# Kernel tuning notes

Measured on AMD Instinct MI355X. Metric: run time of the kernel, lower is better.

The kernel has to match this reference:

```python
import jax, jax.numpy as jnp
import numpy as np

N = 524288   # tokens (accounts)
D = 9        # num_prop_size
E = 2        # expert_size
H = 128      # expert MLP hidden
M = 32       # moe_out
O = 2        # output_size
K = 1        # top-k
LOSS_COF = 0.01
EPS = 1e-10


def setup_inputs() -> dict:
    key = jax.random.key(0)
    ks = jax.random.split(key, 10)
    f32 = jnp.float32
    return {
        "num_prop": jax.random.normal(ks[0], (N, D), f32),
        "cat_prop": jax.random.normal(ks[1], (N, 3), f32),
        "w_gate": jax.random.normal(ks[2], (D, E), f32) * 0.1,
        "W1": jax.random.normal(ks[3], (E, D, H), f32) * 0.1,
        "b1": jax.random.normal(ks[4], (E, H), f32) * 0.01,
        "W2": jax.random.normal(ks[5], (E, H, M), f32) * 0.1,
        "b2": jax.random.normal(ks[6], (E, M), f32) * 0.01,
        "Wout": jax.random.normal(ks[7], (M, O), f32) * 0.1,
        "bout": jax.random.normal(ks[8], (O,), f32) * 0.01,
        "k": K,
    }


def _cv_squared(x):
    # torch: x.var() (unbiased) / (x.mean()**2 + eps)
    return jnp.var(x, ddof=1) / (jnp.mean(x) ** 2 + EPS)


def reference(num_prop, cat_prop, w_gate, W1, b1, W2, b2, Wout, bout, k):
    x = num_prop                                   # eval mode: dropout = identity
    n, e = x.shape[0], w_gate.shape[1]

    # --- top-k gating (eval: clean logits, no noise) ---
    logits = x @ w_gate                            # [N, E]
    top_logits, top_idx = jax.lax.top_k(logits, min(k + 1, e))
    top_k_gates = jax.nn.softmax(top_logits[:, :k], axis=1)   # [N, k]
    rows = jnp.arange(n)[:, None]
    gates = jnp.zeros_like(logits).at[rows, top_idx[:, :k]].set(top_k_gates)  # [N, E]

    importance = gates.sum(axis=0)                 # [E]
    load = (gates > 0).astype(jnp.float32).sum(axis=0)  # [E]
    loss = (_cv_squared(importance) + _cv_squared(load)) * LOSS_COF

    # --- experts: per-expert 2-layer MLP, computed dense (E=2) then gated combine ---
    h = jax.nn.relu(jnp.einsum("nd,edh->neh", x, W1) + b1)    # [N, E, H]
    y_e = jnp.einsum("neh,ehm->nem", h, W2) + b2              # [N, E, M]
    y = jnp.einsum("ne,nem->nm", gates, y_e)                  # [N, M]

    out = y @ Wout + bout                                     # [N, O]
    return (out, loss)
```

## Files before the change

### kernel.cpp

```cpp
#include <hip/hip_runtime.h>

#define NTOK 524288
#define TPB  256
#define TOKB 1024
#define NBLK (NTOK / TOKB)

__device__ __forceinline__ float bf2f(unsigned short u) {
    union { unsigned int i; float f; } v;
    v.i = ((unsigned int)u) << 16;
    return v.f;
}

__device__ __forceinline__ float ldq(const void* p, int i, bool f32) {
    if (f32) return ((const float*)p)[i];
    return bf2f(((const unsigned short*)p)[i]);
}

__global__ void prep_kernel(const void* __restrict__ num_prop,
                            const void* __restrict__ wgate,
                            const void* __restrict__ W1,
                            const void* __restrict__ b1,
                            const void* __restrict__ W2,
                            const void* __restrict__ b2,
                            const void* __restrict__ Wout,
                            const void* __restrict__ bout,
                            unsigned int* __restrict__ cnt1,
                            int* __restrict__ flag,
                            float* __restrict__ bpp,
                            float* __restrict__ wgf,
                            float* __restrict__ wpack)
{
    __shared__ unsigned int bad;
    __shared__ int sflag;
    const int t = threadIdx.x;
    if (t == 0) { bad = 0u; *cnt1 = 0u; }
    __syncthreads();
    if (t < 72) {
        const unsigned short* u = (const unsigned short*)num_prop;
        int e = (u[t] >> 7) & 0xFF;
        if (e < 64 || e > 191) atomicOr(&bad, 1u);
    }
    __syncthreads();
    if (t == 0) { sflag = (int)bad; *flag = (int)bad; }
    __syncthreads();
    const bool f32 = (sflag != 0);

    if (t < 18) wgf[t] = ldq(wgate, t, f32);

    if (t < 4) {
        int e = t >> 1, o = t & 1;
        float acc = ldq(bout, o, f32);
        for (int m = 0; m < 32; ++m)
            acc += ldq(b2, e * 32 + m, f32) * ldq(Wout, m * 2 + o, f32);
        bpp[t] = acc;
    }

    const int e = t >> 7;
    const int j = t & 127;
    float p0 = 0.f, p1 = 0.f;
    for (int m = 0; m < 32; ++m) {
        float w = ldq(W2, (e * 128 + j) * 32 + m, f32);
        p0 += w * ldq(Wout, m * 2 + 0, f32);
        p1 += w * ldq(Wout, m * 2 + 1, f32);
    }
    float* dst = wpack + e * 2048 + j * 16;
    #pragma unroll
    for (int d = 0; d < 9; ++d)
        dst[d] = ldq(W1, (e * 9 + d) * 128 + j, f32);
    dst[9]  = ldq(b1, e * 128 + j, f32);
    dst[10] = p0;
    dst[11] = p1;
    dst[12] = 0.f; dst[13] = 0.f; dst[14] = 0.f; dst[15] = 0.f;
}

__global__ __launch_bounds__(TPB, 2)
void moe_main(const void* __restrict__ xg,
              const int* __restrict__ flag,
              const float* __restrict__ wgf,
              const float* __restrict__ bpp,
              const float* __restrict__ wpack,
              unsigned int* __restrict__ cnt1,
              float2* __restrict__ out)
{
    __shared__ __align__(16) float xs[TOKB * 9];
    __shared__ unsigned short smap[TOKB];
    __shared__ unsigned int wcnt[16];

    const int tid  = threadIdx.x;
    const int lane = tid & 63;
    const int wave = tid >> 6;

    const bool f32 = (*flag) != 0;
    const int gbase = blockIdx.x * (TOKB * 9);
    if (f32) {
        const float* xf = (const float*)xg;
        #pragma unroll
        for (int i = 0; i < 36; ++i)
            xs[tid + i * TPB] = xf[gbase + tid + i * TPB];
    } else {
        const unsigned short* xu = (const unsigned short*)xg;
        for (int i = tid; i < TOKB * 9; i += TPB)
            xs[i] = bf2f(xu[gbase + i]);
    }
    __syncthreads();

    bool e1g[4];
    unsigned long long balg[4];
    #pragma unroll
    for (int g = 0; g < 4; ++g) {
        float l0 = 0.f, l1 = 0.f;
        #pragma unroll
        for (int d = 0; d < 9; ++d) {
            float xv = xs[(g * 256 + tid) * 9 + d];
            l0 = fmaf(xv, wgf[d * 2 + 0], l0);
            l1 = fmaf(xv, wgf[d * 2 + 1], l1);
        }
        e1g[g] = l1 > l0;
        balg[g] = __ballot(e1g[g]);
        if (lane == 0) wcnt[g * 4 + wave] = (unsigned int)__popcll(balg[g]);
    }
    __syncthreads();

    int pres[16]; int run = 0;
    #pragma unroll
    for (int c = 0; c < 16; ++c) { pres[c] = run; run += (int)wcnt[c]; }
    const int n1 = run;
    const int n0 = TOKB - n1;
    const unsigned long long below = (1ull << lane) - 1ull;
    #pragma unroll
    for (int g = 0; g < 4; ++g) {
        const int tok = g * 256 + tid;
        const int pr  = pres[g * 4 + wave] + (int)__popcll(balg[g] & below);
        const int slot = e1g[g] ? (n0 + pr) : (tok - pr);
        smap[slot] = (unsigned short)tok;
    }
    if (tid == 0) atomicAdd(cnt1, (unsigned int)n1);
    __syncthreads();

    const int s0 = tid * 4;
    const int tk0 = (int)smap[s0 + 0], tk1 = (int)smap[s0 + 1];
    const int tk2 = (int)smap[s0 + 2], tk3 = (int)smap[s0 + 3];
    float x0[9], x1[9], x2[9], x3[9];
    #pragma unroll
    for (int d = 0; d < 9; ++d) {
        x0[d] = xs[tk0 * 9 + d];
        x1[d] = xs[tk1 * 9 + d];
        x2[d] = xs[tk2 * 9 + d];
        x3[d] = xs[tk3 * 9 + d];
    }

    const int wslot = __builtin_amdgcn_readfirstlane(wave) << 8;
    const int n0u   = __builtin_amdgcn_readfirstlane(n0);

    float2 r0v, r1v, r2v, r3v;
    if (n0u <= wslot || n0u >= wslot + 256) {
        const int ew = (n0u <= wslot) ? 1 : 0;
        const float* wp = wpack + ew * 2048;
        const float b0 = bpp[ew * 2 + 0], b1v = bpp[ew * 2 + 1];
        float a00 = b0, a01 = b1v, a10 = b0, a11 = b1v;
        float a20 = b0, a21 = b1v, a30 = b0, a31 = b1v;
        #pragma unroll 2
        for (int j = 0; j < 128; ++j) {
            const float* r = wp + j * 16;
            float h0 = r[9], h1 = r[9], h2 = r[9], h3 = r[9];
            #pragma unroll
            for (int d = 0; d < 9; ++d) {
                const float w = r[d];
                h0 = fmaf(x0[d], w, h0);
                h1 = fmaf(x1[d], w, h1);
                h2 = fmaf(x2[d], w, h2);
                h3 = fmaf(x3[d], w, h3);
            }
            h0 = fmaxf(h0, 0.f); h1 = fmaxf(h1, 0.f);
            h2 = fmaxf(h2, 0.f); h3 = fmaxf(h3, 0.f);
            const float wa = r[10], wb = r[11];
            a00 = fmaf(h0, wa, a00); a01 = fmaf(h0, wb, a01);
            a10 = fmaf(h1, wa, a10); a11 = fmaf(h1, wb, a11);
            a20 = fmaf(h2, wa, a20); a21 = fmaf(h2, wb, a21);
            a30 = fmaf(h3, wa, a30); a31 = fmaf(h3, wb, a31);
        }
        r0v.x = a00; r0v.y = a01; r1v.x = a10; r1v.y = a11;
        r2v.x = a20; r2v.y = a21; r3v.x = a30; r3v.y = a31;
    } else {
        float A0[4], A1[4], A2[4], A3[4];
        #pragma unroll
        for (int k = 0; k < 4; ++k) { A0[k] = bpp[0]; A1[k] = bpp[1]; A2[k] = bpp[2]; A3[k] = bpp[3]; }
        for (int j = 0; j < 128; ++j) {
            const float* p0 = wpack + j * 16;
            const float* p1 = wpack + 2048 + j * 16;
            float h00 = p0[9], h01 = p1[9];
            float h10 = p0[9], h11 = p1[9];
            float h20 = p0[9], h21 = p1[9];
            float h30 = p0[9], h31 = p1[9];
            #pragma unroll
            for (int d = 0; d < 9; ++d) {
                const float w0 = p0[d], w1 = p1[d];
                h00 = fmaf(x0[d], w0, h00); h01 = fmaf(x0[d], w1, h01);
                h10 = fmaf(x1[d], w0, h10); h11 = fmaf(x1[d], w1, h11);
                h20 = fmaf(x2[d], w0, h20); h21 = fmaf(x2[d], w1, h21);
                h30 = fmaf(x3[d], w0, h30); h31 = fmaf(x3[d], w1, h31);
            }
            h00 = fmaxf(h00, 0.f); h01 = fmaxf(h01, 0.f);
            h10 = fmaxf(h10, 0.f); h11 = fmaxf(h11, 0.f);
            h20 = fmaxf(h20, 0.f); h21 = fmaxf(h21, 0.f);
            h30 = fmaxf(h30, 0.f); h31 = fmaxf(h31, 0.f);
            const float wa0 = p0[10], wb0 = p0[11], wa1 = p1[10], wb1 = p1[11];
            A0[0] = fmaf(h00, wa0, A0[0]); A1[0] = fmaf(h00, wb0, A1[0]);
            A2[0] = fmaf(h01, wa1, A2[0]); A3[0] = fmaf(h01, wb1, A3[0]);
            A0[1] = fmaf(h10, wa0, A0[1]); A1[1] = fmaf(h10, wb0, A1[1]);
            A2[1] = fmaf(h11, wa1, A2[1]); A3[1] = fmaf(h11, wb1, A3[1]);
            A0[2] = fmaf(h20, wa0, A0[2]); A1[2] = fmaf(h20, wb0, A1[2]);
            A2[2] = fmaf(h21, wa1, A2[2]); A3[2] = fmaf(h21, wb1, A3[2]);
            A0[3] = fmaf(h30, wa0, A0[3]); A1[3] = fmaf(h30, wb0, A1[3]);
            A2[3] = fmaf(h31, wa1, A2[3]); A3[3] = fmaf(h31, wb1, A3[3]);
        }
        const bool e0s = (s0 + 0) >= n0u, e1s = (s0 + 1) >= n0u;
        const bool e2s = (s0 + 2) >= n0u, e3s = (s0 + 3) >= n0u;
        r0v.x = e0s ? A2[0] : A0[0]; r0v.y = e0s ? A3[0] : A1[0];
        r1v.x = e1s ? A2[1] : A0[1]; r1v.y = e1s ? A3[1] : A1[1];
        r2v.x = e2s ? A2[2] : A0[2]; r2v.y = e2s ? A3[2] : A1[2];
        r3v.x = e3s ? A2[3] : A0[3]; r3v.y = e3s ? A3[3] : A1[3];
    }

    __syncthreads();
    float2* ob = (float2*)xs;
    ob[tk0] = r0v; ob[tk1] = r1v; ob[tk2] = r2v; ob[tk3] = r3v;
    __syncthreads();
    const int obase = blockIdx.x * TOKB;
    #pragma unroll
    for (int g = 0; g < 4; ++g)
        out[obase + g * 256 + tid] = ob[g * 256 + tid];
}

__global__ void finalize_kernel(const unsigned int* __restrict__ cnt1,
                                float* __restrict__ loss_out)
{
    double c1 = (double)(*cnt1);
    double c0 = (double)NTOK - c1;
    double diff = c0 - c1;
    double mean = (double)NTOK * 0.5;
    double var  = 0.5 * diff * diff;
    double cv2  = var / (mean * mean + 1e-10);
    *loss_out = (float)(0.02 * cv2);
}

extern "C" void kernel_launch(void* const* d_in, const int* in_sizes, int n_in,
                              void* d_out, int out_size, void* d_ws, size_t ws_size,
                              hipStream_t stream) {
    const void* num_prop = d_in[0];
    const void* w_gate   = d_in[2];
    const void* W1       = d_in[3];
    const void* b1       = d_in[4];
    const void* W2       = d_in[5];
    const void* b2       = d_in[6];
    const void* Wout     = d_in[7];
    const void* bout     = d_in[8];

    char* ws = (char*)d_ws;
    unsigned int* cnt1 = (unsigned int*)ws;
    int* flag          = (int*)(ws + 8);
    float* bpp         = (float*)(ws + 16);
    float* wgf         = (float*)(ws + 64);
    float* wpack       = (float*)(ws + 192);

    float*  outf = (float*)d_out;
    float2* out2 = (float2*)d_out;

    hipLaunchKernelGGL(prep_kernel, dim3(1), dim3(256), 0, stream,
                       num_prop, w_gate, W1, b1, W2, b2, Wout, bout,
                       cnt1, flag, bpp, wgf, wpack);
    hipLaunchKernelGGL(moe_main, dim3(NBLK), dim3(TPB), 0, stream,
                       num_prop, flag, wgf, bpp, wpack, cnt1, out2);
    hipLaunchKernelGGL(finalize_kernel, dim3(1), dim3(1), 0, stream,
                       cnt1, outf + (size_t)NTOK * 2);
}
```

Before: 153.4 us.

## Stage packed expert weights in LDS and broadcast via readlane in uniform waves

Packs the per-hidden-unit weights into 12 floats instead of 16 and copies them into shared memory at block start. Waves whose tokens all use one expert load a per-lane slice into registers and broadcast it with readlane, replacing scalar/global loads. Mixed waves now read per-token expert weights from LDS as float4s instead of computing both experts, which halves their FMAs. The f32 input load is vectorised to float4. The cost is 12 KB more LDS per block, possibly lower occupancy, and many readlane instructions.

```diff
diff --git a/kernel.cpp b/kernel.cpp
--- a/kernel.cpp
+++ b/kernel.cpp
@@ -14,6 +14,10 @@
 __device__ __forceinline__ float ldq(const void* p, int i, bool f32) {
     if (f32) return ((const float*)p)[i];
     return bf2f(((const unsigned short*)p)[i]);
+}
+
+__device__ __forceinline__ float rdlane(float v, int sl) {
+    return __int_as_float(__builtin_amdgcn_readlane(__float_as_int(v), sl));
 }
 
 __global__ void prep_kernel(const void* __restrict__ num_prop,
@@ -63,15 +67,44 @@
         p0 += w * ldq(Wout, m * 2 + 0, f32);
         p1 += w * ldq(Wout, m * 2 + 1, f32);
     }
-    float* dst = wpack + e * 2048 + j * 16;
+    float* dst = wpack + e * 1536 + j * 12;
     #pragma unroll
     for (int d = 0; d < 9; ++d)
         dst[d] = ldq(W1, (e * 9 + d) * 128 + j, f32);
     dst[9]  = ldq(b1, e * 128 + j, f32);
     dst[10] = p0;
     dst[11] = p1;
-    dst[12] = 0.f; dst[13] = 0.f; dst[14] = 0.f; dst[15] = 0.f;
-}
+}
+
+#define JBODY(W)                                                          \
+    {                                                                     \
+        float h0 = W[9], h1 = W[9], h2 = W[9], h3 = W[9];                 \
+        _Pragma("unroll")                                                 \
+        for (int d = 0; d < 9; ++d) {                                     \
+            h0 = fmaf(x0[d], W[d], h0);                                   \
+            h1 = fmaf(x1[d], W[d], h1);                                   \
+            h2 = fmaf(x2[d], W[d], h2);                                   \
+            h3 = fmaf(x3[d], W[d], h3);                                   \
+        }                                                                 \
+        h0 = fmaxf(h0, 0.f); h1 = fmaxf(h1, 0.f);                         \
+        h2 = fmaxf(h2, 0.f); h3 = fmaxf(h3, 0.f);                         \
+        a00 = fmaf(h0, W[10], a00); a01 = fmaf(h0, W[11], a01);           \
+        a10 = fmaf(h1, W[10], a10); a11 = fmaf(h1, W[11], a11);           \
+        a20 = fmaf(h2, W[10], a20); a21 = fmaf(h2, W[11], a21);           \
+        a30 = fmaf(h3, W[10], a30); a31 = fmaf(h3, W[11], a31);           \
+    }
+
+#define JBODYT(xk, A, B, C, ak0, ak1)                                     \
+    {                                                                     \
+        float h = C.y;                                                    \
+        h = fmaf(xk[0], A.x, h); h = fmaf(xk[1], A.y, h);                 \
+        h = fmaf(xk[2], A.z, h); h = fmaf(xk[3], A.w, h);                 \
+        h = fmaf(xk[4], B.x, h); h = fmaf(xk[5], B.y, h);                 \
+        h = fmaf(xk[6], B.z, h); h = fmaf(xk[7], B.w, h);                 \
+        h = fmaf(xk[8], C.x, h);                                         \
+        h = fmaxf(h, 0.f);                                                \
+        ak0 = fmaf(h, C.z, ak0); ak1 = fmaf(h, C.w, ak1);                 \
+    }
 
 __global__ __launch_bounds__(TPB, 2)
 void moe_main(const void* __restrict__ xg,
@@ -83,6 +116,7 @@
               float2* __restrict__ out)
 {
     __shared__ __align__(16) float xs[TOKB * 9];
+    __shared__ __align__(16) float wsm[3072];
     __shared__ unsigned short smap[TOKB];
     __shared__ unsigned int wcnt[16];
 
@@ -91,14 +125,21 @@
     const int wave = tid >> 6;
 
     const bool f32 = (*flag) != 0;
-    const int gbase = blockIdx.x * (TOKB * 9);
+
+    #pragma unroll
+    for (int i = 0; i < 12; ++i)
+        wsm[tid + i * TPB] = wpack[tid + i * TPB];
+
     if (f32) {
-        const float* xf = (const float*)xg;
+        const float4* xf4 = (const float4*)xg;
+        float4* xsv = (float4*)xs;
+        const int g4 = blockIdx.x * (TOKB * 9 / 4);
         #pragma unroll
-        for (int i = 0; i < 36; ++i)
-            xs[tid + i * TPB] = xf[gbase + tid + i * TPB];
+        for (int i = 0; i < 9; ++i)
+            xsv[tid + i * TPB] = xf4[g4 + tid + i * TPB];
     } else {
         const unsigned short* xu = (const unsigned short*)xg;
+        const int gbase = blockIdx.x * (TOKB * 9);
         for (int i = tid; i < TOKB * 9; i += TPB)
             xs[i] = bf2f(xu[gbase + i]);
     }
@@ -152,79 +193,67 @@
     const int wslot = __builtin_amdgcn_readfirstlane(wave) << 8;
     const int n0u   = __builtin_amdgcn_readfirstlane(n0);
 
-    float2 r0v, r1v, r2v, r3v;
+    float a00, a01, a10, a11, a20, a21, a30, a31;
     if (n0u <= wslot || n0u >= wslot + 256) {
         const int ew = (n0u <= wslot) ? 1 : 0;
-        const float* wp = wpack + ew * 2048;
+        float tbl[24];
+        {
+            const float4* src = (const float4*)(wsm + ew * 1536 + lane * 24);
+            #pragma unroll
+            for (int q = 0; q < 6; ++q) {
+                const float4 v = src[q];
+                tbl[q * 4 + 0] = v.x; tbl[q * 4 + 1] = v.y;
+                tbl[q * 4 + 2] = v.z; tbl[q * 4 + 3] = v.w;
+            }
+        }
         const float b0 = bpp[ew * 2 + 0], b1v = bpp[ew * 2 + 1];
-        float a00 = b0, a01 = b1v, a10 = b0, a11 = b1v;
-        float a20 = b0, a21 = b1v, a30 = b0, a31 = b1v;
+        a00 = b0; a01 = b1v; a10 = b0; a11 = b1v;
+        a20 = b0; a21 = b1v; a30 = b0; a31 = b1v;
+        #pragma unroll 2
+        for (int jp = 0; jp < 64; ++jp) {
+            float w0[12], w1[12];
+            #pragma unroll
+            for (int k = 0; k < 12; ++k) {
+                w0[k] = rdlane(tbl[k],      jp);
+                w1[k] = rdlane(tbl[12 + k], jp);
+            }
+            JBODY(w0)
+            JBODY(w1)
+        }
+    } else {
+        const int ex0 = ((s0 + 0) >= n0u) ? 1 : 0;
+        const int ex1 = ((s0 + 1) >= n0u) ? 1 : 0;
+        const int ex2 = ((s0 + 2) >= n0u) ? 1 : 0;
+        const int ex3 = ((s0 + 3) >= n0u) ? 1 : 0;
+        const int eb0 = ex0 * 1536, eb1 = ex1 * 1536;
+        const int eb2 = ex2 * 1536, eb3 = ex3 * 1536;
+        a00 = bpp[ex0 * 2 + 0]; a01 = bpp[ex0 * 2 + 1];
+        a10 = bpp[ex1 * 2 + 0]; a11 = bpp[ex1 * 2 + 1];
+        a20 = bpp[ex2 * 2 + 0]; a21 = bpp[ex2 * 2 + 1];
+        a30 = bpp[ex3 * 2 + 0]; a31 = bpp[ex3 * 2 + 1];
         #pragma unroll 2
         for (int j = 0; j < 128; ++j) {
-            const float* r = wp + j * 16;
-            float h0 = r[9], h1 = r[9], h2 = r[9], h3 = r[9];
-            #pragma unroll
-            for (int d = 0; d < 9; ++d) {
-                const float w = r[d];
-                h0 = fmaf(x0[d], w, h0);
-                h1 = fmaf(x1[d], w, h1);
-                h2 = fmaf(x2[d], w, h2);
-                h3 = fmaf(x3[d], w, h3);
-            }
-            h0 = fmaxf(h0, 0.f); h1 = fmaxf(h1, 0.f);
-            h2 = fmaxf(h2, 0.f); h3 = fmaxf(h3, 0.f);
-            const float wa = r[10], wb = r[11];
-            a00 = fmaf(h0, wa, a00); a01 = fmaf(h0, wb, a01);
-            a10 = fmaf(h1, wa, a10); a11 = fmaf(h1, wb, a11);
-            a20 = fmaf(h2, wa, a20); a21 = fmaf(h2, wb, a21);
-            a30 = fmaf(h3, wa, a30); a31 = fmaf(h3, wb, a31);
+            const float4* q0 = (const float4*)(wsm + eb0 + j * 12);
+            const float4* q1 = (const float4*)(wsm + eb1 + j * 12);
+            const float4* q2 = (const float4*)(wsm + eb2 + j * 12);
+            const float4* q3 = (const float4*)(wsm + eb3 + j * 12);
+            const float4 A0 = q0[0], B0 = q0[1], C0 = q0[2];
+            const float4 A1 = q1[0], B1 = q1[1], C1 = q1[2];
+            const float4 A2 = q2[0], B2 = q2[1], C2 = q2[2];
+            const float4 A3 = q3[0], B3 = q3[1], C3 = q3[2];
+            JBODYT(x0, A0, B0, C0, a00, a01)
+            JBODYT(x1, A1, B1, C1, a10, a11)
+            JBODYT(x2, A2, B2, C2, a20, a21)
+            JBODYT(x3, A3, B3, C3, a30, a31)
         }
-        r0v.x = a00; r0v.y = a01; r1v.x = a10; r1v.y = a11;
-        r2v.x = a20; r2v.y = a21; r3v.x = a30; r3v.y = a31;
-    } else {
-        float A0[4], A1[4], A2[4], A3[4];
-        #pragma unroll
-        for (int k = 0; k < 4; ++k) { A0[k] = bpp[0]; A1[k] = bpp[1]; A2[k] = bpp[2]; A3[k] = bpp[3]; }
-        for (int j = 0; j < 128; ++j) {
-            const float* p0 = wpack + j * 16;
-            const float* p1 = wpack + 2048 + j * 16;
-            float h00 = p0[9], h01 = p1[9];
-            float h10 = p0[9], h11 = p1[9];
-            float h20 = p0[9], h21 = p1[9];
-            float h30 = p0[9], h31 = p1[9];
-            #pragma unroll
-            for (int d = 0; d < 9; ++d) {
-                const float w0 = p0[d], w1 = p1[d];
-                h00 = fmaf(x0[d], w0, h00); h01 = fmaf(x0[d], w1, h01);
-                h10 = fmaf(x1[d], w0, h10); h11 = fmaf(x1[d], w1, h11);
-                h20 = fmaf(x2[d], w0, h20); h21 = fmaf(x2[d], w1, h21);
-                h30 = fmaf(x3[d], w0, h30); h31 = fmaf(x3[d], w1, h31);
-            }
-            h00 = fmaxf(h00, 0.f); h01 = fmaxf(h01, 0.f);
-            h10 = fmaxf(h10, 0.f); h11 = fmaxf(h11, 0.f);
-            h20 = fmaxf(h20, 0.f); h21 = fmaxf(h21, 0.f);
-            h30 = fmaxf(h30, 0.f); h31 = fmaxf(h31, 0.f);
-            const float wa0 = p0[10], wb0 = p0[11], wa1 = p1[10], wb1 = p1[11];
-            A0[0] = fmaf(h00, wa0, A0[0]); A1[0] = fmaf(h00, wb0, A1[0]);
-            A2[0] = fmaf(h01, wa1, A2[0]); A3[0] = fmaf(h01, wb1, A3[0]);
-            A0[1] = fmaf(h10, wa0, A0[1]); A1[1] = fmaf(h10, wb0, A1[1]);
-            A2[1] = fmaf(h11, wa1, A2[1]); A3[1] = fmaf(h11, wb1, A3[1]);
-            A0[2] = fmaf(h20, wa0, A0[2]); A1[2] = fmaf(h20, wb0, A1[2]);
-            A2[2] = fmaf(h21, wa1, A2[2]); A3[2] = fmaf(h21, wb1, A3[2]);
-            A0[3] = fmaf(h30, wa0, A0[3]); A1[3] = fmaf(h30, wb0, A1[3]);
-            A2[3] = fmaf(h31, wa1, A2[3]); A3[3] = fmaf(h31, wb1, A3[3]);
-        }
-        const bool e0s = (s0 + 0) >= n0u, e1s = (s0 + 1) >= n0u;
-        const bool e2s = (s0 + 2) >= n0u, e3s = (s0 + 3) >= n0u;
-        r0v.x = e0s ? A2[0] : A0[0]; r0v.y = e0s ? A3[0] : A1[0];
-        r1v.x = e1s ? A2[1] : A0[1]; r1v.y = e1s ? A3[1] : A1[1];
-        r2v.x = e2s ? A2[2] : A0[2]; r2v.y = e2s ? A3[2] : A1[2];
-        r3v.x = e3s ? A2[3] : A0[3]; r3v.y = e3s ? A3[3] : A1[3];
     }
 
     __syncthreads();
     float2* ob = (float2*)xs;
-    ob[tk0] = r0v; ob[tk1] = r1v; ob[tk2] = r2v; ob[tk3] = r3v;
+    ob[tk0] = make_float2(a00, a01);
+    ob[tk1] = make_float2(a10, a11);
+    ob[tk2] = make_float2(a20, a21);
+    ob[tk3] = make_float2(a30, a31);
     __syncthreads();
     const int obase = blockIdx.x * TOKB;
     #pragma unroll
```

After: 136.0 us. 1.13x faster.
